# Kernel optimization log

Measured on AMD Instinct MI355X. Metric: run time of the kernel, lower is better.

The kernel has to match this reference:

```python
import jax, jax.numpy as jnp
import numpy as np

N_LAYERS = 6
D_MODEL = 512
D_FFN = 2048
N_STATE = 64
KSIZE = 31
BATCH = 8
SEQ = 2048
IN_SIZE = 80


def _ln(x, g, b, eps=1e-5):
    m = jnp.mean(x, axis=-1, keepdims=True)
    v = jnp.mean((x - m) ** 2, axis=-1, keepdims=True)
    return (x - m) * jax.lax.rsqrt(v + eps) * g + b


def _ffn(x, g, b, w1, b1, w2, b2):
    # LayerNorm -> Linear(D->F) -> GELU -> Linear(F->D)  (PositionalwiseFeedForward)
    h = jax.nn.gelu(_ln(x, g, b) @ w1 + b1)
    return h @ w2 + b2


def _dss(x, lam_re, lam_im, c_re, c_im, d_skip, log_dt, w_out, b_out):
    # Diagonal state-space (DSS-EXP): generate length-T kernel from diagonal poles,
    # apply causal conv via FFT, skip D*u, GELU, GLU output projection.
    Bx, T, H = x.shape
    dt = jnp.exp(log_dt)
    lam = -jnp.exp(lam_re) + 1j * lam_im                        # [N] stable poles (Re<0)
    P = jnp.exp(lam[:, None] * (dt * jnp.arange(T))[None, :])   # [N, T]
    C = c_re + 1j * c_im                                        # [H, N]
    kern = jnp.einsum('hn,nt->ht', C, P).real * dt              # [H, T]
    u = x.transpose(0, 2, 1)                                    # [B, H, T]
    n = 2 * T
    y = jnp.fft.irfft(jnp.fft.rfft(u, n=n) * jnp.fft.rfft(kern, n=n), n=n)[..., :T]
    y = y + d_skip[None, :, None] * u
    y = jax.nn.gelu(y.transpose(0, 2, 1))                       # [B, T, H]
    z = y @ w_out + b_out                                       # [B, T, 2H]
    a, g = jnp.split(z, 2, axis=-1)
    return a * jax.nn.sigmoid(g)                                # GLU


def _conv_module(x, g1, b1, bw, bb, dw, db, g2, b2, lw, lb):
    # LN -> 1x1 conv to 2D + GLU -> depthwise conv (SAME, k=31) -> LN -> GELU -> Linear
    y = _ln(x, g1, b1)
    y = y @ bw.T + bb                                           # [B, T, 2D]
    a, g = jnp.split(y, 2, axis=-1)
    y = a * jax.nn.sigmoid(g)                                   # GLU over channels
    yc = y.transpose(0, 2, 1)                                   # [B, D, T]
    yc = jax.lax.conv_general_dilated(
        yc, dw[:, None, :], (1,), 'SAME',
        feature_group_count=yc.shape[1],
        dimension_numbers=('NCH', 'OIH', 'NCH'))
    yc = yc + db[None, :, None]
    y = jax.nn.gelu(_ln(yc.transpose(0, 2, 1), g2, b2))
    return y @ lw.T + lb


def _forward(src, speaker_embs, src_w, src_b,
             ffn1_ln_g, ffn1_ln_b, ffn1_w1, ffn1_b1, ffn1_w2, ffn1_b2,
             norm1_g, norm1_b,
             lam_re, lam_im, c_re, c_im, ssm_d, log_dt, dss_out_w, dss_out_b,
             conv_ln_g, conv_ln_b, bneck_w, bneck_b, dw_w, dw_b,
             conv_ln2_g, conv_ln2_b, conv_lin_w, conv_lin_b,
             ffn2_ln_g, ffn2_ln_b, ffn2_w1, ffn2_b1, ffn2_w2, ffn2_b2,
             norm2_g, norm2_b, final_g, final_b):
    x = src @ src_w + src_b                                     # custom_src_module Linear
    for i in range(N_LAYERS):
        x = x + 0.5 * _ffn(x, ffn1_ln_g[i], ffn1_ln_b[i], ffn1_w1[i], ffn1_b1[i], ffn1_w2[i], ffn1_b2[i])
        skip = x
        x = _ln(x, norm1_g[i], norm1_b[i])
        x = _dss(x, lam_re[i], lam_im[i], c_re[i], c_im[i], ssm_d[i], log_dt[i], dss_out_w[i], dss_out_b[i])
        x = x + skip
        x = x + _conv_module(x, conv_ln_g[i], conv_ln_b[i], bneck_w[i], bneck_b[i], dw_w[i], dw_b[i],
                             conv_ln2_g[i], conv_ln2_b[i], conv_lin_w[i], conv_lin_b[i])
        x = _ln(x + 0.5 * _ffn(x, ffn2_ln_g[i], ffn2_ln_b[i], ffn2_w1[i], ffn2_b1[i], ffn2_w2[i], ffn2_b2[i]),
                norm2_g[i], norm2_b[i])
    x = _ln(x, final_g, final_b, eps=1e-6)
    return x + speaker_embs


def setup_inputs() -> dict:
    key = jax.random.key(0)
    ks = iter(jax.random.split(key, 64))
    def rn(shape, s=0.02):
        return (jax.random.normal(next(ks), shape) * s).astype(jnp.float32)
    L, D, F, N, K = N_LAYERS, D_MODEL, D_FFN, N_STATE, KSIZE
    return dict(
        src=jax.random.normal(next(ks), (BATCH, SEQ, IN_SIZE), dtype=jnp.float32),
        speaker_embs=jax.random.normal(next(ks), (BATCH, 1, D), dtype=jnp.float32),
        src_w=rn((IN_SIZE, D)), src_b=jnp.zeros((D,), jnp.float32),
        ffn1_ln_g=jnp.ones((L, D), jnp.float32), ffn1_ln_b=jnp.zeros((L, D), jnp.float32),
        ffn1_w1=rn((L, D, F)), ffn1_b1=jnp.zeros((L, F), jnp.float32),
        ffn1_w2=rn((L, F, D)), ffn1_b2=jnp.zeros((L, D), jnp.float32),
        norm1_g=jnp.ones((L, D), jnp.float32), norm1_b=jnp.zeros((L, D), jnp.float32),
        lam_re=rn((L, N), 0.5), lam_im=rn((L, N), 3.0),
        c_re=rn((L, D, N), 0.1), c_im=rn((L, D, N), 0.1),
        ssm_d=rn((L, D), 1.0), log_dt=jnp.full((L,), float(np.log(0.01)), jnp.float32),
        dss_out_w=rn((L, D, 2 * D)), dss_out_b=jnp.zeros((L, 2 * D), jnp.float32),
        conv_ln_g=jnp.ones((L, D), jnp.float32), conv_ln_b=jnp.zeros((L, D), jnp.float32),
        bneck_w=rn((L, 2 * D, D)), bneck_b=jnp.zeros((L, 2 * D), jnp.float32),
        dw_w=rn((L, D, K), 0.1), dw_b=jnp.zeros((L, D), jnp.float32),
        conv_ln2_g=jnp.ones((L, D), jnp.float32), conv_ln2_b=jnp.zeros((L, D), jnp.float32),
        conv_lin_w=rn((L, D, D)), conv_lin_b=jnp.zeros((L, D), jnp.float32),
        ffn2_ln_g=jnp.ones((L, D), jnp.float32), ffn2_ln_b=jnp.zeros((L, D), jnp.float32),
        ffn2_w1=rn((L, D, F)), ffn2_b1=jnp.zeros((L, F), jnp.float32),
        ffn2_w2=rn((L, F, D)), ffn2_b2=jnp.zeros((L, D), jnp.float32),
        norm2_g=jnp.ones((L, D), jnp.float32), norm2_b=jnp.zeros((L, D), jnp.float32),
        final_g=jnp.ones((D,), jnp.float32), final_b=jnp.zeros((D,), jnp.float32),
    )


def reference(src, speaker_embs, src_w, src_b,
              ffn1_ln_g, ffn1_ln_b, ffn1_w1, ffn1_b1, ffn1_w2, ffn1_b2,
              norm1_g, norm1_b,
              lam_re, lam_im, c_re, c_im, ssm_d, log_dt, dss_out_w, dss_out_b,
              conv_ln_g, conv_ln_b, bneck_w, bneck_b, dw_w, dw_b,
              conv_ln2_g, conv_ln2_b, conv_lin_w, conv_lin_b,
              ffn2_ln_g, ffn2_ln_b, ffn2_w1, ffn2_b1, ffn2_w2, ffn2_b2,
              norm2_g, norm2_b, final_g, final_b):
    return _forward(src, speaker_embs, src_w, src_b,
                    ffn1_ln_g, ffn1_ln_b, ffn1_w1, ffn1_b1, ffn1_w2, ffn1_b2,
                    norm1_g, norm1_b,
                    lam_re, lam_im, c_re, c_im, ssm_d, log_dt, dss_out_w, dss_out_b,
                    conv_ln_g, conv_ln_b, bneck_w, bneck_b, dw_w, dw_b,
                    conv_ln2_g, conv_ln2_b, conv_lin_w, conv_lin_b,
                    ffn2_ln_g, ffn2_ln_b, ffn2_w1, ffn2_b1, ffn2_w2, ffn2_b2,
                    norm2_g, norm2_b, final_g, final_b)
```

## Files before the change

kernel.cpp:

```cpp
#include <hip/hip_runtime.h>
#include <hip/hip_bf16.h>
#include <stdint.h>


#define NL 6
#define TT 2048
#define BB 8
#define DD 512
#define FF 2048
#define ROWS (BB*TT)

typedef __attribute__((ext_vector_type(4))) float f32x4;
typedef __attribute__((ext_vector_type(8))) short s16x8;

#define DEVI __device__ __forceinline__

DEVI float bf2f(uint32_t u) { union { uint32_t i; float f; } v; v.i = u << 16; return v.f; }
DEVI uint16_t f2bf(float f) {
    union { float f; uint32_t i; } v; v.f = f;
    uint32_t x = v.i;
    return (uint16_t)((x + 0x7fffu + ((x >> 16) & 1u)) >> 16);
}
DEVI float gelu_f(float x) {
    float x2 = x * x;
    float z  = x * fmaf(x2, 0.07135481627f, 1.5957691216f);
    return x * __builtin_amdgcn_rcpf(1.0f + __expf(-z));
}
DEVI float sigm(float x) { return __builtin_amdgcn_rcpf(1.0f + __expf(-x)); }

DEVI void gload16(const uint16_t* g, uint16_t* l) {
    __builtin_amdgcn_global_load_lds((const __attribute__((address_space(1))) void*)g,
                                     (__attribute__((address_space(3))) void*)l, 16, 0, 0);
}

__global__ void k_wtrans(const float* __restrict__ src, uint16_t* __restrict__ dst,
                         int K, int N) {
    __shared__ float tile[32][33];
    int l = blockIdx.z;
    const float* s = src + (size_t)l * K * N;
    uint16_t*    d = dst + (size_t)l * N * K;
    int n0 = blockIdx.x * 32, k0 = blockIdx.y * 32;
    int tx = threadIdx.x, ty = threadIdx.y;
#pragma unroll
    for (int i = 0; i < 4; i++) {
        int k = k0 + ty + i * 8;
        tile[ty + i * 8][tx] = s[(size_t)k * N + n0 + tx];
    }
    __syncthreads();
#pragma unroll
    for (int i = 0; i < 4; i++) {
        int n = n0 + ty + i * 8;
        d[(size_t)n * K + k0 + tx] = f2bf(tile[tx][ty + i * 8]);
    }
}
__global__ void k_wcvt(const float* __restrict__ src, uint16_t* __restrict__ dst, int n) {
    int i = blockIdx.x * 256 + threadIdx.x;
    if (i < n) dst[i] = f2bf(src[i]);
}
__global__ void k_dwt(const float* __restrict__ dw, float* __restrict__ dwt) {
    int i = blockIdx.x * 256 + threadIdx.x;
    int tot = NL * DD * 31;
    if (i >= tot) return;
    int l = i / (DD * 31), r = i % (DD * 31), d = r / 31, k = r % 31;
    dwt[(size_t)l * 31 * DD + k * DD + d] = dw[i];
}
__global__ void k_srcpad(const float* __restrict__ src, uint16_t* __restrict__ dst) {
    int i = blockIdx.x * 256 + threadIdx.x;
    if (i >= ROWS * 128) return;
    int r = i >> 7, c = i & 127;
    dst[i] = (c < 80) ? f2bf(src[(size_t)r * 80 + c]) : (uint16_t)0;
}
__global__ void k_wsrcpad(const float* __restrict__ w, uint16_t* __restrict__ dst) {
    int i = blockIdx.x * 256 + threadIdx.x;
    if (i >= DD * 128) return;
    int n = i >> 7, k = i & 127;
    dst[i] = (k < 80) ? f2bf(w[(size_t)k * DD + n]) : (uint16_t)0;
}

template <int MODE>
__global__ void k_ln(const float* __restrict__ in, void* __restrict__ outp,
                     const float* __restrict__ gam, const float* __restrict__ bet,
                     const float* __restrict__ spk, float eps) {
    int row  = blockIdx.x * 4 + (threadIdx.x >> 6);
    int lane = threadIdx.x & 63;
    const float* x = in + (size_t)row * DD;
    float4 a0 = *(const float4*)&x[lane * 4];
    float4 a1 = *(const float4*)&x[256 + lane * 4];
    float v[8] = {a0.x, a0.y, a0.z, a0.w, a1.x, a1.y, a1.z, a1.w};
    float s = 0.f, q = 0.f;
#pragma unroll
    for (int i = 0; i < 8; i++) { s += v[i]; q += v[i] * v[i]; }
#pragma unroll
    for (int m = 1; m < 64; m <<= 1) { s += __shfl_xor(s, m); q += __shfl_xor(q, m); }
    float mean = s * (1.0f / 512.0f);
    float var  = fmaxf(q * (1.0f / 512.0f) - mean * mean, 0.0f);
    float inv  = rsqrtf(var + eps);
    float4 g0 = *(const float4*)&gam[lane * 4];
    float4 g1 = *(const float4*)&gam[256 + lane * 4];
    float4 b0 = *(const float4*)&bet[lane * 4];
    float4 b1 = *(const float4*)&bet[256 + lane * 4];
    float gv[8] = {g0.x, g0.y, g0.z, g0.w, g1.x, g1.y, g1.z, g1.w};
    float bv[8] = {b0.x, b0.y, b0.z, b0.w, b1.x, b1.y, b1.z, b1.w};
    float y[8];
#pragma unroll
    for (int i = 0; i < 8; i++) y[i] = (v[i] - mean) * inv * gv[i] + bv[i];
    uint16_t* o = (uint16_t*)outp + (size_t)row * DD;
    uint2 p0, p1;
    p0.x = (uint32_t)f2bf(y[0]) | ((uint32_t)f2bf(y[1]) << 16);
    p0.y = (uint32_t)f2bf(y[2]) | ((uint32_t)f2bf(y[3]) << 16);
    p1.x = (uint32_t)f2bf(y[4]) | ((uint32_t)f2bf(y[5]) << 16);
    p1.y = (uint32_t)f2bf(y[6]) | ((uint32_t)f2bf(y[7]) << 16);
    *(uint2*)&o[lane * 4]       = p0;
    *(uint2*)&o[256 + lane * 4] = p1;
}

template <int M2>
__global__ void k_ln2(const float* __restrict__ in, float* __restrict__ X,
                      void* __restrict__ out2,
                      const float* __restrict__ g1, const float* __restrict__ b1,
                      const float* __restrict__ g2, const float* __restrict__ b2,
                      const float* __restrict__ spk, float eps2) {
    int row  = blockIdx.x * 4 + (threadIdx.x >> 6);
    int lane = threadIdx.x & 63;
    const float* x = in + (size_t)row * DD;
    float4 a0 = *(const float4*)&x[lane * 4];
    float4 a1 = *(const float4*)&x[256 + lane * 4];
    float v[8] = {a0.x, a0.y, a0.z, a0.w, a1.x, a1.y, a1.z, a1.w};
    float s = 0.f, q = 0.f;
#pragma unroll
    for (int i = 0; i < 8; i++) { s += v[i]; q += v[i] * v[i]; }
#pragma unroll
    for (int m = 1; m < 64; m <<= 1) { s += __shfl_xor(s, m); q += __shfl_xor(q, m); }
    float mean = s * (1.0f / 512.0f);
    float var  = fmaxf(q * (1.0f / 512.0f) - mean * mean, 0.0f);
    float inv  = rsqrtf(var + 1e-5f);
    float4 g0 = *(const float4*)&g1[lane * 4];
    float4 g1v = *(const float4*)&g1[256 + lane * 4];
    float4 b0 = *(const float4*)&b1[lane * 4];
    float4 b1v = *(const float4*)&b1[256 + lane * 4];
    float gv[8] = {g0.x, g0.y, g0.z, g0.w, g1v.x, g1v.y, g1v.z, g1v.w};
    float bv[8] = {b0.x, b0.y, b0.z, b0.w, b1v.x, b1v.y, b1v.z, b1v.w};
    float y[8];
    float s2 = 0.f, q2 = 0.f;
#pragma unroll
    for (int i = 0; i < 8; i++) {
        y[i] = (v[i] - mean) * inv * gv[i] + bv[i];
        s2 += y[i]; q2 += y[i] * y[i];
    }
    if (M2 == 6) {
        float* xo = X + (size_t)row * DD;
        *(float4*)&xo[lane * 4]       = make_float4(y[0], y[1], y[2], y[3]);
        *(float4*)&xo[256 + lane * 4] = make_float4(y[4], y[5], y[6], y[7]);
    }
#pragma unroll
    for (int m = 1; m < 64; m <<= 1) { s2 += __shfl_xor(s2, m); q2 += __shfl_xor(q2, m); }
    float mean2 = s2 * (1.0f / 512.0f);
    float var2  = fmaxf(q2 * (1.0f / 512.0f) - mean2 * mean2, 0.0f);
    float inv2  = rsqrtf(var2 + eps2);
    float4 G0 = *(const float4*)&g2[lane * 4];
    float4 G1 = *(const float4*)&g2[256 + lane * 4];
    float4 B0 = *(const float4*)&b2[lane * 4];
    float4 B1v = *(const float4*)&b2[256 + lane * 4];
    float Gv[8] = {G0.x, G0.y, G0.z, G0.w, G1.x, G1.y, G1.z, G1.w};
    float Bv[8] = {B0.x, B0.y, B0.z, B0.w, B1v.x, B1v.y, B1v.z, B1v.w};
    float z[8];
#pragma unroll
    for (int i = 0; i < 8; i++) z[i] = (y[i] - mean2) * inv2 * Gv[i] + Bv[i];
    if (M2 == 6) {
        uint16_t* o = (uint16_t*)out2 + (size_t)row * DD;
        uint2 p0, p1;
        p0.x = (uint32_t)f2bf(z[0]) | ((uint32_t)f2bf(z[1]) << 16);
        p0.y = (uint32_t)f2bf(z[2]) | ((uint32_t)f2bf(z[3]) << 16);
        p1.x = (uint32_t)f2bf(z[4]) | ((uint32_t)f2bf(z[5]) << 16);
        p1.y = (uint32_t)f2bf(z[6]) | ((uint32_t)f2bf(z[7]) << 16);
        *(uint2*)&o[lane * 4]       = p0;
        *(uint2*)&o[256 + lane * 4] = p1;
    } else {
        const float* sp = spk + (size_t)(row >> 11) * DD;
        float4 s0 = *(const float4*)&sp[lane * 4];
        float4 s1 = *(const float4*)&sp[256 + lane * 4];
        float* o = (float*)out2 + (size_t)row * DD;
        *(float4*)&o[lane * 4]       = make_float4(z[0]+s0.x, z[1]+s0.y, z[2]+s0.z, z[3]+s0.w);
        *(float4*)&o[256 + lane * 4] = make_float4(z[4]+s1.x, z[5]+s1.y, z[6]+s1.z, z[7]+s1.w);
    }
}

__global__ void k_gluln(const uint16_t* __restrict__ H, float* __restrict__ X,
                        uint16_t* __restrict__ out,
                        const float* __restrict__ gam, const float* __restrict__ bet) {
    int row  = blockIdx.x * 4 + (threadIdx.x >> 6);
    int lane = threadIdx.x & 63;
    const uint16_t* hr = H + (size_t)row * 1024;
    uint2 ha0 = *(const uint2*)&hr[lane * 4];
    uint2 ha1 = *(const uint2*)&hr[256 + lane * 4];
    uint2 hg0 = *(const uint2*)&hr[512 + lane * 4];
    uint2 hg1 = *(const uint2*)&hr[768 + lane * 4];
    uint32_t aw[4] = {ha0.x, ha0.y, ha1.x, ha1.y};
    uint32_t gw[4] = {hg0.x, hg0.y, hg1.x, hg1.y};
    float* xr = X + (size_t)row * DD;
    float4 x0 = *(const float4*)&xr[lane * 4];
    float4 x1 = *(const float4*)&xr[256 + lane * 4];
    float xv[8] = {x0.x, x0.y, x0.z, x0.w, x1.x, x1.y, x1.z, x1.w};
    float v[8];
#pragma unroll
    for (int p = 0; p < 4; p++) {
        float a0 = bf2f(aw[p] & 0xffffu), a1 = bf2f(aw[p] >> 16);
        float g0 = bf2f(gw[p] & 0xffffu), g1 = bf2f(gw[p] >> 16);
        v[2*p]   = xv[2*p]   + a0 * sigm(g0);
        v[2*p+1] = xv[2*p+1] + a1 * sigm(g1);
    }
    *(float4*)&xr[lane * 4]       = make_float4(v[0], v[1], v[2], v[3]);
    *(float4*)&xr[256 + lane * 4] = make_float4(v[4], v[5], v[6], v[7]);
    float s = 0.f, q = 0.f;
#pragma unroll
    for (int i = 0; i < 8; i++) { s += v[i]; q += v[i] * v[i]; }
#pragma unroll
    for (int m = 1; m < 64; m <<= 1) { s += __shfl_xor(s, m); q += __shfl_xor(q, m); }
    float mean = s * (1.0f / 512.0f);
    float var  = fmaxf(q * (1.0f / 512.0f) - mean * mean, 0.0f);
    float inv  = rsqrtf(var + 1e-5f);
    float4 g0 = *(const float4*)&gam[lane * 4];
    float4 g1 = *(const float4*)&gam[256 + lane * 4];
    float4 b0 = *(const float4*)&bet[lane * 4];
    float4 b1 = *(const float4*)&bet[256 + lane * 4];
    float gv[8] = {g0.x, g0.y, g0.z, g0.w, g1.x, g1.y, g1.z, g1.w};
    float bv[8] = {b0.x, b0.y, b0.z, b0.w, b1.x, b1.y, b1.z, b1.w};
    uint16_t* o = out + (size_t)row * DD;
    uint2 p0, p1;
    float y0 = (v[0]-mean)*inv*gv[0]+bv[0], y1 = (v[1]-mean)*inv*gv[1]+bv[1];
    float y2 = (v[2]-mean)*inv*gv[2]+bv[2], y3 = (v[3]-mean)*inv*gv[3]+bv[3];
    float y4 = (v[4]-mean)*inv*gv[4]+bv[4], y5 = (v[5]-mean)*inv*gv[5]+bv[5];
    float y6 = (v[6]-mean)*inv*gv[6]+bv[6], y7 = (v[7]-mean)*inv*gv[7]+bv[7];
    p0.x = (uint32_t)f2bf(y0) | ((uint32_t)f2bf(y1) << 16);
    p0.y = (uint32_t)f2bf(y2) | ((uint32_t)f2bf(y3) << 16);
    p1.x = (uint32_t)f2bf(y4) | ((uint32_t)f2bf(y5) << 16);
    p1.y = (uint32_t)f2bf(y6) | ((uint32_t)f2bf(y7) << 16);
    *(uint2*)&o[lane * 4]       = p0;
    *(uint2*)&o[256 + lane * 4] = p1;
}

template <int MODE, int WM, int WN, int BN>
__global__ __launch_bounds__(512) void k_gemm2(
    const uint16_t* __restrict__ A, const uint16_t* __restrict__ Bt,
    const float* __restrict__ bias, int M, int N, int K,
    void* __restrict__ outp, float* __restrict__ X) {
    constexpr int BM = 256;
    constexpr int MR = BM / WM / 16;
    constexpr int NR = BN / WN / 16;
    constexpr int ABLK = (BM / 16) * 2;
    constexpr int BBLK = (BN / 16) * 2;
    constexpr int APW = ABLK / 8;
    constexpr int BPW = BBLK / 8;
    __shared__ __align__(16) uint16_t As[2][ABLK * 512];
    __shared__ __align__(16) uint16_t Bs[2][BBLK * 512];
    int tid = threadIdx.x;
    int wave = tid >> 6, lane = tid & 63;
    int l15 = lane & 15, l16 = lane >> 4;
    int wr = wave / WN, wc = wave % WN;
    int m0 = blockIdx.x * BM, n0 = blockIdx.y * BN;

    const uint16_t* srcA[APW];
    const uint16_t* srcB[BPW];
#pragma unroll
    for (int p = 0; p < APW; p++) {
        int bi = wave * APW + p, rb = bi >> 1, ks = bi & 1;
        srcA[p] = A + (size_t)(m0 + rb * 16 + l15) * K + ks * 32 + l16 * 8;
    }
#pragma unroll
    for (int p = 0; p < BPW; p++) {
        int bi = wave * BPW + p, rb = bi >> 1, ks = bi & 1;
        srcB[p] = Bt + (size_t)(n0 + rb * 16 + l15) * K + ks * 32 + l16 * 8;
    }

    f32x4 acc[MR][NR];
#pragma unroll
    for (int i = 0; i < MR; i++)
#pragma unroll
        for (int j = 0; j < NR; j++) acc[i][j] = (f32x4){0.f, 0.f, 0.f, 0.f};

#pragma unroll
    for (int p = 0; p < APW; p++) gload16(srcA[p], &As[0][(wave * APW + p) * 512]);
#pragma unroll
    for (int p = 0; p < BPW; p++) gload16(srcB[p], &Bs[0][(wave * BPW + p) * 512]);
    __syncthreads();

    int nk = K >> 6;
    for (int it = 0; it < nk; ++it) {
        int cur = it & 1;
        if (it + 1 < nk) {
            int kt = (it + 1) << 6;
#pragma unroll
            for (int p = 0; p < APW; p++)
                gload16(srcA[p] + kt, &As[cur ^ 1][(wave * APW + p) * 512]);
#pragma unroll
            for (int p = 0; p < BPW; p++)
                gload16(srcB[p] + kt, &Bs[cur ^ 1][(wave * BPW + p) * 512]);
        }
#pragma unroll
        for (int s = 0; s < 2; s++) {
            s16x8 af[MR], bfr[NR];
#pragma unroll
            for (int i = 0; i < MR; i++)
                af[i] = *(const s16x8*)&As[cur][((wr * MR + i) * 2 + s) * 512 + lane * 8];
#pragma unroll
            for (int j = 0; j < NR; j++)
                bfr[j] = *(const s16x8*)&Bs[cur][((wc * NR + j) * 2 + s) * 512 + lane * 8];
#pragma unroll
            for (int i = 0; i < MR; i++)
#pragma unroll
                for (int j = 0; j < NR; j++)
                    acc[i][j] = __builtin_amdgcn_mfma_f32_16x16x32_bf16(af[i], bfr[j], acc[i][j], 0, 0, 0);
        }
        __syncthreads();
    }
#pragma unroll
    for (int i = 0; i < MR; i++) {
#pragma unroll
        for (int j = 0; j < NR; j++) {
            int gcol = n0 + wc * NR * 16 + j * 16 + l15;
            float bv = bias[gcol];
#pragma unroll
            for (int q = 0; q < 4; q++) {
                int grow = m0 + wr * MR * 16 + i * 16 + l16 * 4 + q;
                float v = acc[i][j][q] + bv;
                if (MODE == 0) {
                    ((uint16_t*)outp)[(size_t)grow * N + gcol] = f2bf(gelu_f(v));
                } else if (MODE == 1) {
                    ((uint16_t*)outp)[(size_t)grow * N + gcol] = f2bf(v);
                } else if (MODE == 2) {
                    X[(size_t)grow * DD + gcol] += 0.5f * v;
                } else if (MODE == 3) {
                    X[(size_t)grow * DD + gcol] += v;
                } else if (MODE == 4) {
                    ((float*)outp)[(size_t)grow * DD + gcol] =
                        X[(size_t)grow * DD + gcol] + 0.5f * v;
                } else {
                    X[(size_t)grow * DD + gcol] = v;
                }
            }
        }
    }
}

__global__ void k_tpose(const uint16_t* __restrict__ in, uint16_t* __restrict__ out,
                        int R, int C) {
    __shared__ uint16_t tile[32][33];
    size_t boff = (size_t)blockIdx.z * R * C;
    int c0 = blockIdx.x * 32, r0 = blockIdx.y * 32;
    int tx = threadIdx.x, ty = threadIdx.y;
#pragma unroll
    for (int i = 0; i < 4; i++)
        tile[ty + i * 8][tx] = in[boff + (size_t)(r0 + ty + i * 8) * C + c0 + tx];
    __syncthreads();
#pragma unroll
    for (int i = 0; i < 4; i++)
        out[boff + (size_t)(c0 + ty + i * 8) * R + r0 + tx] = tile[tx][ty + i * 8];
}

__global__ __launch_bounds__(64) void k_phiprep(
        const float* __restrict__ lam_re, const float* __restrict__ lam_im,
        const float* __restrict__ log_dt, uint16_t* __restrict__ PHI,
        float* __restrict__ A64f) {
    int l = blockIdx.x, n = threadIdx.x;
    float dt = expf(log_dt[l]);
    float lr = lam_re[l * 64 + n], li = lam_im[l * 64 + n];
    float mag = expf(-expf(lr) * dt), th = li * dt;
    float Are = mag * __cosf(th), Aim = mag * __sinf(th);
    float Pre = 1.f, Pim = 0.f;
    uint16_t* ph = PHI + (size_t)l * 8192;
    for (int tau = 0; tau < 64; tau++) {
        int s = 63 - tau;
        ph[n * 64 + s]        = f2bf(Pre);
        ph[(64 + n) * 64 + s] = f2bf(Pim);
        float nr = Pre * Are - Pim * Aim;
        float ni = Pre * Aim + Pim * Are;
        Pre = nr; Pim = ni;
    }
    A64f[l * 128 + 2 * n]     = Pre;
    A64f[l * 128 + 2 * n + 1] = Pim;
}

__global__ __launch_bounds__(64) void k_gprep(
        const float* __restrict__ lam_re, const float* __restrict__ lam_im,
        const float* __restrict__ c_re, const float* __restrict__ c_im,
        const float* __restrict__ ssm_d, const float* __restrict__ log_dt,
        int l, uint16_t* __restrict__ G) {
    int h = blockIdx.x, n = threadIdx.x;
    __shared__ float klds[64];
    float dt = expf(log_dt[l]);
    float lr = lam_re[l * 64 + n], li = lam_im[l * 64 + n];
    float mag = expf(-expf(lr) * dt), th = li * dt;
    float Are = mag * __cosf(th), Aim = mag * __sinf(th);
    float Cre = c_re[(size_t)l * DD * 64 + h * 64 + n];
    float Cim = c_im[(size_t)l * DD * 64 + h * 64 + n];
    uint16_t* Gh = G + (size_t)h * 64 * 192;
    float Pre = 1.f, Pim = 0.f;
    for (int r = 0; r < 64; r++) {
        float t = Cre * Pre - Cim * Pim;
        float s = t;
        s += __shfl_xor(s, 1);  s += __shfl_xor(s, 2);  s += __shfl_xor(s, 4);
        s += __shfl_xor(s, 8);  s += __shfl_xor(s, 16); s += __shfl_xor(s, 32);
        if (n == 0) klds[r] = dt * s;
        float nr = Pre * Are - Pim * Aim;
        float ni = Pre * Aim + Pim * Are;
        float wre = dt * (Cre * nr - Cim * ni);
        float wim = dt * (Cre * ni + Cim * nr);
        Gh[r * 192 + 64 + n]  = f2bf(wre);
        Gh[r * 192 + 128 + n] = f2bf(-wim);
        Pre = nr; Pim = ni;
    }
    __syncthreads();
    float dh = ssm_d[l * DD + h];
    for (int r = 0; r < 64; r++) {
        int c = n;
        float val = (c < r) ? klds[r - c] : (c == r ? klds[0] + dh : 0.f);
        Gh[r * 192 + c] = f2bf(val);
    }
}

__global__ __launch_bounds__(256) void k_pass1(
        const uint16_t* __restrict__ u, const uint16_t* __restrict__ PHI,
        uint16_t* __restrict__ E) {
    __shared__ __align__(16) uint16_t Phs[128 * 72];
    int tid = threadIdx.x;
    for (int v = tid; v < 1024; v += 256) {
        int row = v >> 3, kb = v & 7;
        *(s16x8*)&Phs[row * 72 + kb * 8] = *(const s16x8*)&PHI[row * 64 + kb * 8];
    }
    __syncthreads();
    int wave = tid >> 6, lane = tid & 63;
    int l15 = lane & 15, l16 = lane >> 4;
    int m0 = (wave & 1) * 64;
    int colbase = blockIdx.x * 128 + (wave >> 1) * 64;
    f32x4 acc[4][4];
#pragma unroll
    for (int i = 0; i < 4; i++)
#pragma unroll
        for (int j = 0; j < 4; j++) acc[i][j] = (f32x4){0.f, 0.f, 0.f, 0.f};
#pragma unroll
    for (int kt = 0; kt < 64; kt += 32) {
        s16x8 a[4], b[4];
#pragma unroll
        for (int i = 0; i < 4; i++)
            a[i] = *(const s16x8*)&Phs[(m0 + i * 16 + l15) * 72 + kt + l16 * 8];
#pragma unroll
        for (int j = 0; j < 4; j++)
            b[j] = *(const s16x8*)(u + (size_t)(colbase + j * 16 + l15) * 64 + kt + l16 * 8);
#pragma unroll
        for (int i = 0; i < 4; i++)
#pragma unroll
            for (int j = 0; j < 4; j++)
                acc[i][j] = __builtin_amdgcn_mfma_f32_16x16x32_bf16(a[i], b[j], acc[i][j], 0, 0, 0);
    }
#pragma unroll
    for (int i = 0; i < 4; i++)
#pragma unroll
        for (int j = 0; j < 4; j++) {
            int col = colbase + j * 16 + l15;
            int r0  = m0 + i * 16 + l16 * 4;
            uint32_t p0 = (uint32_t)f2bf(acc[i][j][0]) | ((uint32_t)f2bf(acc[i][j][1]) << 16);
            uint32_t p1 = (uint32_t)f2bf(acc[i][j][2]) | ((uint32_t)f2bf(acc[i][j][3]) << 16);
            *(uint2*)&E[(size_t)col * 128 + r0] = make_uint2(p0, p1);
        }
}

__global__ void k_pass2(const uint16_t* __restrict__ E, const float* __restrict__ A64f,
                        int l, uint16_t* __restrict__ Sp) {
    int gid = blockIdx.x * 256 + threadIdx.x;
    int n = gid & 63, bh = gid >> 6;
    int b = bh >> 9, h = bh & 511;
    float2 A = *(const float2*)&A64f[l * 128 + 2 * n];
    float Sre = 0.f, Sim = 0.f;
    const uint16_t* Eb = E + (size_t)bh * 32 * 128;
    uint16_t* So = Sp + (size_t)h * 32768 + (size_t)b * 32 * 128;
    for (int i = 0; i < 32; i++) {
        So[i * 128 + n]      = f2bf(Sre);
        So[i * 128 + 64 + n] = f2bf(Sim);
        float er = bf2f((uint32_t)Eb[i * 128 + n]);
        float ei = bf2f((uint32_t)Eb[i * 128 + 64 + n]);
        float nr = A.x * Sre - A.y * Sim + er;
        float ni = A.x * Sim + A.y * Sre + ei;
        Sre = nr; Sim = ni;
    }
}

__global__ __launch_bounds__(256) void k_pass3(
        const uint16_t* __restrict__ G, const uint16_t* __restrict__ u,
        const uint16_t* __restrict__ Sp, uint16_t* __restrict__ Y) {
    __shared__ __align__(16) uint16_t Gs[64 * 200];
    int h = blockIdx.x, tid = threadIdx.x;
    for (int v = tid; v < 1536; v += 256) {
        int row = v / 24, kb = v % 24;
        *(s16x8*)&Gs[row * 200 + kb * 8] = *(const s16x8*)&G[(size_t)h * 12288 + row * 192 + kb * 8];
    }
    __syncthreads();
    int wave = tid >> 6, lane = tid & 63;
    int l15 = lane & 15, l16 = lane >> 4;
    int wn = wave * 64;
    const uint16_t* uh = u + (size_t)h * TT;
    const uint16_t* sh = Sp + (size_t)h * 32768;
    f32x4 acc[4][4];
#pragma unroll
    for (int i = 0; i < 4; i++)
#pragma unroll
        for (int j = 0; j < 4; j++) acc[i][j] = (f32x4){0.f, 0.f, 0.f, 0.f};
#pragma unroll
    for (int kt = 0; kt < 192; kt += 32) {
        s16x8 a[4], b[4];
#pragma unroll
        for (int i = 0; i < 4; i++)
            a[i] = *(const s16x8*)&Gs[(i * 16 + l15) * 200 + kt + l16 * 8];
#pragma unroll
        for (int j = 0; j < 4; j++) {
            int col = wn + j * 16 + l15;
            const uint16_t* src;
            if (kt < 64)
                src = uh + (size_t)(col >> 5) * (DD * TT) + (col & 31) * 64 + kt + l16 * 8;
            else
                src = sh + (size_t)col * 128 + (kt - 64) + l16 * 8;
            b[j] = *(const s16x8*)src;
        }
#pragma unroll
        for (int i = 0; i < 4; i++)
#pragma unroll
            for (int j = 0; j < 4; j++)
                acc[i][j] = __builtin_amdgcn_mfma_f32_16x16x32_bf16(a[i], b[j], acc[i][j], 0, 0, 0);
    }
#pragma unroll
    for (int i = 0; i < 4; i++)
#pragma unroll
        for (int j = 0; j < 4; j++) {
            int col = wn + j * 16 + l15;
            int r0  = i * 16 + l16 * 4;
            uint16_t* dst = Y + (size_t)(col >> 5) * (DD * TT) + (size_t)h * TT + (col & 31) * 64 + r0;
            uint32_t p0 = (uint32_t)f2bf(acc[i][j][0]) | ((uint32_t)f2bf(acc[i][j][1]) << 16);
            uint32_t p1 = (uint32_t)f2bf(acc[i][j][2]) | ((uint32_t)f2bf(acc[i][j][3]) << 16);
            *(uint2*)&dst[0] = make_uint2(p0, p1);
        }
}

__global__ void k_tgelu(const uint16_t* __restrict__ y, uint16_t* __restrict__ out) {
    __shared__ uint16_t tile[32][33];
    int b = blockIdx.z;
    int t0 = blockIdx.x * 32, h0 = blockIdx.y * 32;
    int tx = threadIdx.x, ty = threadIdx.y;
    const uint16_t* yb = y + (size_t)b * DD * TT;
#pragma unroll
    for (int i = 0; i < 4; i++) {
        int h = h0 + ty + i * 8;
        tile[ty + i * 8][tx] = f2bf(gelu_f(bf2f((uint32_t)yb[(size_t)h * TT + t0 + tx])));
    }
    __syncthreads();
    uint16_t* ob = out + (size_t)b * TT * DD;
#pragma unroll
    for (int i = 0; i < 4; i++) {
        int t = t0 + ty + i * 8;
        ob[(size_t)t * DD + h0 + tx] = tile[tx][ty + i * 8];
    }
}

__global__ void k_glu(const uint16_t* __restrict__ z, uint16_t* __restrict__ out) {
    int i = blockIdx.x * 256 + threadIdx.x;
    int r = i >> 8;
    int c = (i & 255) * 2;
    uint32_t av = *(const uint32_t*)&z[(size_t)r * 1024 + c];
    uint32_t gv = *(const uint32_t*)&z[(size_t)r * 1024 + 512 + c];
    float a0 = bf2f(av & 0xffffu), a1 = bf2f(av >> 16);
    float g0 = bf2f(gv & 0xffffu), g1 = bf2f(gv >> 16);
    float v0 = a0 * sigm(g0), v1 = a1 * sigm(g1);
    uint32_t p = (uint32_t)f2bf(v0) | ((uint32_t)f2bf(v1) << 16);
    *(uint32_t*)&out[(size_t)r * DD + c] = p;
}

__global__ __launch_bounds__(256) void k_dwln(
        const uint16_t* __restrict__ in, const float* __restrict__ dwt,
        const float* __restrict__ db, const float* __restrict__ gam,
        const float* __restrict__ bet, uint16_t* __restrict__ out) {
    __shared__ __align__(16) uint16_t xs[34 * 512];
    __shared__ float red[4][4][2];
    int tid = threadIdx.x;
    int t0 = (blockIdx.x & 511) * 4;
    int b  = blockIdx.x >> 9;
    const uint16_t* ib = in + (size_t)b * TT * DD;
    for (int v = tid; v < 34 * 64; v += 256) {
        int row = v >> 6, seg = v & 63;
        int tj = t0 - 15 + row;
        uint4 val = make_uint4(0, 0, 0, 0);
        if (tj >= 0 && tj < TT) val = *(const uint4*)&ib[(size_t)tj * DD + seg * 8];
        *(uint4*)&xs[row * 512 + seg * 8] = val;
    }
    __syncthreads();
    int d = tid * 2;
    int wave = tid >> 6, lane = tid & 63;
    float a0[4], a1[4];
    float bv0 = db[d], bv1 = db[d + 1];
#pragma unroll
    for (int o = 0; o < 4; o++) { a0[o] = bv0; a1[o] = bv1; }
#pragma unroll
    for (int k = 0; k < 31; k++) {
        float2 w = *(const float2*)&dwt[k * DD + d];
#pragma unroll
        for (int o = 0; o < 4; o++) {
            uint32_t v = *(const uint32_t*)&xs[(o + k) * 512 + d];
            a0[o] = fmaf(bf2f(v & 0xffffu), w.x, a0[o]);
            a1[o] = fmaf(bf2f(v >> 16), w.y, a1[o]);
        }
    }
#pragma unroll
    for (int o = 0; o < 4; o++) {
        float ss = a0[o] + a1[o];
        float qq = a0[o] * a0[o] + a1[o] * a1[o];
#pragma unroll
        for (int m = 1; m < 64; m <<= 1) { ss += __shfl_xor(ss, m); qq += __shfl_xor(qq, m); }
        if (lane == 0) { red[o][wave][0] = ss; red[o][wave][1] = qq; }
    }
    __syncthreads();
    float g0 = gam[d], g1 = gam[d + 1], be0 = bet[d], be1 = bet[d + 1];
#pragma unroll
    for (int o = 0; o < 4; o++) {
        float s = red[o][0][0] + red[o][1][0] + red[o][2][0] + red[o][3][0];
        float q = red[o][0][1] + red[o][1][1] + red[o][2][1] + red[o][3][1];
        float mean = s * (1.0f / 512.0f);
        float var  = fmaxf(q * (1.0f / 512.0f) - mean * mean, 0.0f);
        float inv  = rsqrtf(var + 1e-5f);
        float y0 = gelu_f((a0[o] - mean) * inv * g0 + be0);
        float y1 = gelu_f((a1[o] - mean) * inv * g1 + be1);
        uint32_t p = (uint32_t)f2bf(y0) | ((uint32_t)f2bf(y1) << 16);
        *(uint32_t*)&out[((size_t)b * TT + t0 + o) * DD + d] = p;
    }
}

extern "C" void kernel_launch(void* const* d_in, const int* in_sizes, int n_in,
                              void* d_out, int out_size, void* d_ws, size_t ws_size,
                              hipStream_t stream) {
    const float* src        = (const float*)d_in[0];
    const float* speaker    = (const float*)d_in[1];
    const float* src_w      = (const float*)d_in[2];
    const float* src_b      = (const float*)d_in[3];
    const float* ffn1_ln_g  = (const float*)d_in[4];
    const float* ffn1_ln_b  = (const float*)d_in[5];
    const float* ffn1_w1    = (const float*)d_in[6];
    const float* ffn1_b1    = (const float*)d_in[7];
    const float* ffn1_w2    = (const float*)d_in[8];
    const float* ffn1_b2    = (const float*)d_in[9];
    const float* norm1_g    = (const float*)d_in[10];
    const float* norm1_b    = (const float*)d_in[11];
    const float* lam_re     = (const float*)d_in[12];
    const float* lam_im     = (const float*)d_in[13];
    const float* c_re       = (const float*)d_in[14];
    const float* c_im       = (const float*)d_in[15];
    const float* ssm_d      = (const float*)d_in[16];
    const float* log_dt     = (const float*)d_in[17];
    const float* dss_out_w  = (const float*)d_in[18];
    const float* dss_out_b  = (const float*)d_in[19];
    const float* conv_ln_g  = (const float*)d_in[20];
    const float* conv_ln_b  = (const float*)d_in[21];
    const float* bneck_w    = (const float*)d_in[22];
    const float* bneck_b    = (const float*)d_in[23];
    const float* dw_w       = (const float*)d_in[24];
    const float* dw_b       = (const float*)d_in[25];
    const float* conv_ln2_g = (const float*)d_in[26];
    const float* conv_ln2_b = (const float*)d_in[27];
    const float* conv_lin_w = (const float*)d_in[28];
    const float* conv_lin_b = (const float*)d_in[29];
    const float* ffn2_ln_g  = (const float*)d_in[30];
    const float* ffn2_ln_b  = (const float*)d_in[31];
    const float* ffn2_w1    = (const float*)d_in[32];
    const float* ffn2_b1    = (const float*)d_in[33];
    const float* ffn2_w2    = (const float*)d_in[34];
    const float* ffn2_b2    = (const float*)d_in[35];
    const float* norm2_g    = (const float*)d_in[36];
    const float* norm2_b    = (const float*)d_in[37];
    const float* final_g    = (const float*)d_in[38];
    const float* final_b    = (const float*)d_in[39];
    (void)in_sizes; (void)n_in; (void)out_size; (void)ws_size;

    uint8_t* ws = (uint8_t*)d_ws;
    float*    X   = (float*)   (ws + 0);
    float*    F0  = (float*)   (ws + 33554432);
    uint16_t* B1  = (uint16_t*)(ws + 67108864);
    uint16_t* B2  = (uint16_t*)(ws + 83886080);
    uint16_t* B3  = (uint16_t*)(ws + 100663296);
    uint16_t* H   = (uint16_t*)(ws + 117440512);
    uint16_t* Wf1a= (uint16_t*)(ws + 184549376);
    uint16_t* Wf1b= (uint16_t*)(ws + 197132288);
    uint16_t* Wds = (uint16_t*)(ws + 209715200);
    uint16_t* Wbn = (uint16_t*)(ws + 216006656);
    uint16_t* Wcl = (uint16_t*)(ws + 222298112);
    uint16_t* Wf2a= (uint16_t*)(ws + 225443840);
    uint16_t* Wf2b= (uint16_t*)(ws + 238026752);
    float*    DWT = (float*)   (ws + 250609664);
    uint16_t* PHI = (uint16_t*)(ws + 250990592);
    float*    A64f= (float*)   (ws + 251088896);

    uint16_t* GBUF = B1;
    uint16_t* SPK  = (uint16_t*)F0;
    uint16_t* EBUF = H;
    uint16_t* SRCB = B3;
    uint16_t* WSRC = B2;

    dim3 tb(32, 8);
    k_wtrans<<<dim3(FF/32, DD/32, NL), tb, 0, stream>>>(ffn1_w1, Wf1a, DD, FF);
    k_wtrans<<<dim3(DD/32, FF/32, NL), tb, 0, stream>>>(ffn1_w2, Wf1b, FF, DD);
    k_wtrans<<<dim3(1024/32, DD/32, NL), tb, 0, stream>>>(dss_out_w, Wds, DD, 1024);
    k_wcvt<<<(NL*1024*DD + 255)/256, 256, 0, stream>>>(bneck_w, Wbn, NL*1024*DD);
    k_wcvt<<<(NL*DD*DD + 255)/256, 256, 0, stream>>>(conv_lin_w, Wcl, NL*DD*DD);
    k_wtrans<<<dim3(FF/32, DD/32, NL), tb, 0, stream>>>(ffn2_w1, Wf2a, DD, FF);
    k_wtrans<<<dim3(DD/32, FF/32, NL), tb, 0, stream>>>(ffn2_w2, Wf2b, FF, DD);
    k_dwt<<<(NL*DD*31 + 255)/256, 256, 0, stream>>>(dw_w, DWT);
    k_phiprep<<<NL, 64, 0, stream>>>(lam_re, lam_im, log_dt, PHI, A64f);
    k_srcpad<<<(ROWS*128 + 255)/256, 256, 0, stream>>>(src, SRCB);
    k_wsrcpad<<<(DD*128 + 255)/256, 256, 0, stream>>>(src_w, WSRC);

    k_gemm2<5,4,2,128><<<dim3(64, 4), 512, 0, stream>>>(SRCB, WSRC, src_b, ROWS, DD, 128, nullptr, X);
    k_ln<0><<<4096, 256, 0, stream>>>(X, B1, ffn1_ln_g, ffn1_ln_b, nullptr, 1e-5f);

    for (int l = 0; l < NL; l++) {
        k_gemm2<0,2,4,256><<<dim3(64, 8), 512, 0, stream>>>(B1, Wf1a + (size_t)l*FF*DD, ffn1_b1 + l*FF,
                                                            ROWS, FF, DD, H, nullptr);
        k_gemm2<2,4,2,128><<<dim3(64, 4), 512, 0, stream>>>(H, Wf1b + (size_t)l*DD*FF, ffn1_b2 + l*DD,
                                                            ROWS, DD, FF, nullptr, X);
        k_ln<0><<<4096, 256, 0, stream>>>(X, B1, norm1_g + l*DD, norm1_b + l*DD, nullptr, 1e-5f);
        k_tpose<<<dim3(DD/32, TT/32, BB), tb, 0, stream>>>(B1, B2, TT, DD);
        k_gprep<<<DD, 64, 0, stream>>>(lam_re, lam_im, c_re, c_im, ssm_d, log_dt, l, GBUF);
        k_pass1<<<1024, 256, 0, stream>>>(B2, PHI + (size_t)l*8192, EBUF);
        k_pass2<<<1024, 256, 0, stream>>>(EBUF, A64f, l, SPK);
        k_pass3<<<DD, 256, 0, stream>>>(GBUF, B2, SPK, B3);
        k_tgelu<<<dim3(TT/32, DD/32, BB), tb, 0, stream>>>(B3, B1);
        k_gemm2<1,2,4,256><<<dim3(64, 4), 512, 0, stream>>>(B1, Wds + (size_t)l*1024*DD, dss_out_b + l*1024,
                                                            ROWS, 1024, DD, H, nullptr);
        k_gluln<<<4096, 256, 0, stream>>>(H, X, B1, conv_ln_g + l*DD, conv_ln_b + l*DD);
        k_gemm2<1,2,4,256><<<dim3(64, 4), 512, 0, stream>>>(B1, Wbn + (size_t)l*1024*DD, bneck_b + l*1024,
                                                            ROWS, 1024, DD, H, nullptr);
        k_glu<<<ROWS, 256, 0, stream>>>(H, B2);
        k_dwln<<<BB*512, 256, 0, stream>>>(B2, DWT + (size_t)l*31*DD, dw_b + l*DD,
                                           conv_ln2_g + l*DD, conv_ln2_b + l*DD, B1);
        k_gemm2<3,4,2,128><<<dim3(64, 4), 512, 0, stream>>>(B1, Wcl + (size_t)l*DD*DD, conv_lin_b + l*DD,
                                                            ROWS, DD, DD, nullptr, X);
        k_ln<0><<<4096, 256, 0, stream>>>(X, B1, ffn2_ln_g + l*DD, ffn2_ln_b + l*DD, nullptr, 1e-5f);
        k_gemm2<0,2,4,256><<<dim3(64, 8), 512, 0, stream>>>(B1, Wf2a + (size_t)l*FF*DD, ffn2_b1 + l*FF,
                                                            ROWS, FF, DD, H, nullptr);
        k_gemm2<4,4,2,128><<<dim3(64, 4), 512, 0, stream>>>(H, Wf2b + (size_t)l*DD*FF, ffn2_b2 + l*DD,
                                                            ROWS, DD, FF, F0, X);
        if (l < NL - 1) {
            k_ln2<6><<<4096, 256, 0, stream>>>(F0, X, B1, norm2_g + l*DD, norm2_b + l*DD,
                                               ffn1_ln_g + (l+1)*DD, ffn1_ln_b + (l+1)*DD,
                                               nullptr, 1e-5f);
        } else {
            k_ln2<7><<<4096, 256, 0, stream>>>(F0, nullptr, d_out, norm2_g + l*DD, norm2_b + l*DD,
                                               final_g, final_b, speaker, 1e-6f);
        }
    }
}
```

Before: 3.403 ms.

## Rewrite GEMM with triple-buffered K=32 pipeline and XCD-aware block swizzle

Replaces the double-buffered K=64 GEMM with a triple-buffered K=32 pipeline. It uses explicit vmcnt waits and a single barrier per step, so global loads run two stages ahead of the MFMA work. Work-group IDs are remapped across the eight XCDs so neighbouring tiles share L2, and launch bounds now request two blocks per CU. The warp layout is fixed at 2x4 with 8 M-fragments per wave, which raises register pressure. The hand-set vmcnt counts depend on how many loads each stage issues and are easy to get wrong.

Result: slower. 3.657 ms (+7.5%).

```diff
diff --git a/kernel.cpp b/kernel.cpp
--- a/kernel.cpp
+++ b/kernel.cpp
@@ -239,37 +239,43 @@
     *(uint2*)&o[256 + lane * 4] = p1;
 }
 
-template <int MODE, int WM, int WN, int BN>
-__global__ __launch_bounds__(512) void k_gemm2(
+template <int MODE, int BN>
+__global__ __launch_bounds__(512, 2) void k_gemm3(
     const uint16_t* __restrict__ A, const uint16_t* __restrict__ Bt,
     const float* __restrict__ bias, int M, int N, int K,
     void* __restrict__ outp, float* __restrict__ X) {
-    constexpr int BM = 256;
-    constexpr int MR = BM / WM / 16;
-    constexpr int NR = BN / WN / 16;
-    constexpr int ABLK = (BM / 16) * 2;
-    constexpr int BBLK = (BN / 16) * 2;
-    constexpr int APW = ABLK / 8;
+    constexpr int MR = 8;
+    constexpr int NR = BN / 64;
+    constexpr int ABLK = 16;
+    constexpr int BBLK = BN / 16;
+    constexpr int APW = 2;
     constexpr int BPW = BBLK / 8;
-    __shared__ __align__(16) uint16_t As[2][ABLK * 512];
-    __shared__ __align__(16) uint16_t Bs[2][BBLK * 512];
+    constexpr int LV  = APW + BPW;
+    __shared__ __align__(16) uint16_t As[3][ABLK * 512];
+    __shared__ __align__(16) uint16_t Bs[3][BBLK * 512];
     int tid = threadIdx.x;
     int wave = tid >> 6, lane = tid & 63;
     int l15 = lane & 15, l16 = lane >> 4;
-    int wr = wave / WN, wc = wave % WN;
-    int m0 = blockIdx.x * BM, n0 = blockIdx.y * BN;
+    int wr = wave >> 2, wc = wave & 3;
+
+    int nwg = gridDim.x;
+    int q8  = nwg >> 3;
+    int wg  = (blockIdx.x & 7) * q8 + (blockIdx.x >> 3);
+    int nbx = M >> 8;
+    int bx = wg % nbx, by = wg / nbx;
+    int m0 = bx * 256, n0 = by * BN;
 
     const uint16_t* srcA[APW];
     const uint16_t* srcB[BPW];
 #pragma unroll
     for (int p = 0; p < APW; p++) {
-        int bi = wave * APW + p, rb = bi >> 1, ks = bi & 1;
-        srcA[p] = A + (size_t)(m0 + rb * 16 + l15) * K + ks * 32 + l16 * 8;
+        int bi = wave * APW + p;
+        srcA[p] = A + (size_t)(m0 + bi * 16 + l15) * K + l16 * 8;
     }
 #pragma unroll
     for (int p = 0; p < BPW; p++) {
-        int bi = wave * BPW + p, rb = bi >> 1, ks = bi & 1;
-        srcB[p] = Bt + (size_t)(n0 + rb * 16 + l15) * K + ks * 32 + l16 * 8;
+        int bi = wave * BPW + p;
+        srcB[p] = Bt + (size_t)(n0 + bi * 16 + l15) * K + l16 * 8;
     }
 
     f32x4 acc[MR][NR];
@@ -278,40 +284,43 @@
 #pragma unroll
         for (int j = 0; j < NR; j++) acc[i][j] = (f32x4){0.f, 0.f, 0.f, 0.f};
 
-#pragma unroll
-    for (int p = 0; p < APW; p++) gload16(srcA[p], &As[0][(wave * APW + p) * 512]);
-#pragma unroll
-    for (int p = 0; p < BPW; p++) gload16(srcB[p], &Bs[0][(wave * BPW + p) * 512]);
-    __syncthreads();
-
-    int nk = K >> 6;
-    for (int it = 0; it < nk; ++it) {
-        int cur = it & 1;
-        if (it + 1 < nk) {
-            int kt = (it + 1) << 6;
-#pragma unroll
-            for (int p = 0; p < APW; p++)
-                gload16(srcA[p] + kt, &As[cur ^ 1][(wave * APW + p) * 512]);
-#pragma unroll
-            for (int p = 0; p < BPW; p++)
-                gload16(srcB[p] + kt, &Bs[cur ^ 1][(wave * BPW + p) * 512]);
+    auto STAGE = [&](int tt) {
+        int b = tt % 3;
+        int kof = tt << 5;
+#pragma unroll
+        for (int p = 0; p < APW; p++)
+            gload16(srcA[p] + kof, &As[b][(wave * APW + p) * 512]);
+#pragma unroll
+        for (int p = 0; p < BPW; p++)
+            gload16(srcB[p] + kof, &Bs[b][(wave * BPW + p) * 512]);
+    };
+
+    int nk = K >> 5;
+    STAGE(0);
+    STAGE(1);
+    for (int t = 0; t < nk; ++t) {
+        if (t + 1 < nk) {
+            if (LV == 4) asm volatile("s_waitcnt vmcnt(4)" ::: "memory");
+            else         asm volatile("s_waitcnt vmcnt(3)" ::: "memory");
+        } else {
+            asm volatile("s_waitcnt vmcnt(0)" ::: "memory");
         }
-#pragma unroll
-        for (int s = 0; s < 2; s++) {
-            s16x8 af[MR], bfr[NR];
-#pragma unroll
-            for (int i = 0; i < MR; i++)
-                af[i] = *(const s16x8*)&As[cur][((wr * MR + i) * 2 + s) * 512 + lane * 8];
+        __builtin_amdgcn_s_barrier();
+        asm volatile("" ::: "memory");
+        if (t + 2 < nk) STAGE(t + 2);
+        int buf = t % 3;
+        s16x8 af[MR], bfr[NR];
+#pragma unroll
+        for (int i = 0; i < MR; i++)
+            af[i] = *(const s16x8*)&As[buf][(wr * MR + i) * 512 + lane * 8];
+#pragma unroll
+        for (int j = 0; j < NR; j++)
+            bfr[j] = *(const s16x8*)&Bs[buf][(wc * NR + j) * 512 + lane * 8];
+#pragma unroll
+        for (int i = 0; i < MR; i++)
 #pragma unroll
             for (int j = 0; j < NR; j++)
-                bfr[j] = *(const s16x8*)&Bs[cur][((wc * NR + j) * 2 + s) * 512 + lane * 8];
-#pragma unroll
-            for (int i = 0; i < MR; i++)
-#pragma unroll
-                for (int j = 0; j < NR; j++)
-                    acc[i][j] = __builtin_amdgcn_mfma_f32_16x16x32_bf16(af[i], bfr[j], acc[i][j], 0, 0, 0);
-        }
-        __syncthreads();
+                acc[i][j] = __builtin_amdgcn_mfma_f32_16x16x32_bf16(af[i], bfr[j], acc[i][j], 0, 0, 0);
     }
 #pragma unroll
     for (int i = 0; i < MR; i++) {
@@ -712,14 +721,14 @@
     k_srcpad<<<(ROWS*128 + 255)/256, 256, 0, stream>>>(src, SRCB);
     k_wsrcpad<<<(DD*128 + 255)/256, 256, 0, stream>>>(src_w, WSRC);
 
-    k_gemm2<5,4,2,128><<<dim3(64, 4), 512, 0, stream>>>(SRCB, WSRC, src_b, ROWS, DD, 128, nullptr, X);
+    k_gemm3<5,128><<<256, 512, 0, stream>>>(SRCB, WSRC, src_b, ROWS, DD, 128, nullptr, X);
     k_ln<0><<<4096, 256, 0, stream>>>(X, B1, ffn1_ln_g, ffn1_ln_b, nullptr, 1e-5f);
 
     for (int l = 0; l < NL; l++) {
-        k_gemm2<0,2,4,256><<<dim3(64, 8), 512, 0, stream>>>(B1, Wf1a + (size_t)l*FF*DD, ffn1_b1 + l*FF,
-                                                            ROWS, FF, DD, H, nullptr);
-        k_gemm2<2,4,2,128><<<dim3(64, 4), 512, 0, stream>>>(H, Wf1b + (size_t)l*DD*FF, ffn1_b2 + l*DD,
-                                                            ROWS, DD, FF, nullptr, X);
+        k_gemm3<0,256><<<512, 512, 0, stream>>>(B1, Wf1a + (size_t)l*FF*DD, ffn1_b1 + l*FF,
+                                                ROWS, FF, DD, H, nullptr);
+        k_gemm3<2,128><<<256, 512, 0, stream>>>(H, Wf1b + (size_t)l*DD*FF, ffn1_b2 + l*DD,
+                                                ROWS, DD, FF, nullptr, X);
         k_ln<0><<<4096, 256, 0, stream>>>(X, B1, norm1_g + l*DD, norm1_b + l*DD, nullptr, 1e-5f);
         k_tpose<<<dim3(DD/32, TT/32, BB), tb, 0, stream>>>(B1, B2, TT, DD);
         k_gprep<<<DD, 64, 0, stream>>>(lam_re, lam_im, c_re, c_im, ssm_d, log_dt, l, GBUF);
@@ -727,21 +736,21 @@
         k_pass2<<<1024, 256, 0, stream>>>(EBUF, A64f, l, SPK);
         k_pass3<<<DD, 256, 0, stream>>>(GBUF, B2, SPK, B3);
         k_tgelu<<<dim3(TT/32, DD/32, BB), tb, 0, stream>>>(B3, B1);
-        k_gemm2<1,2,4,256><<<dim3(64, 4), 512, 0, stream>>>(B1, Wds + (size_t)l*1024*DD, dss_out_b + l*1024,
-                                                            ROWS, 1024, DD, H, nullptr);
+        k_gemm3<1,256><<<256, 512, 0, stream>>>(B1, Wds + (size_t)l*1024*DD, dss_out_b + l*1024,
+                                                ROWS, 1024, DD, H, nullptr);
         k_gluln<<<4096, 256, 0, stream>>>(H, X, B1, conv_ln_g + l*DD, conv_ln_b + l*DD);
-        k_gemm2<1,2,4,256><<<dim3(64, 4), 512, 0, stream>>>(B1, Wbn + (size_t)l*1024*DD, bneck_b + l*1024,
-                                                            ROWS, 1024, DD, H, nullptr);
+        k_gemm3<1,256><<<256, 512, 0, stream>>>(B1, Wbn + (size_t)l*1024*DD, bneck_b + l*1024,
+                                                ROWS, 1024, DD, H, nullptr);
         k_glu<<<ROWS, 256, 0, stream>>>(H, B2);
         k_dwln<<<BB*512, 256, 0, stream>>>(B2, DWT + (size_t)l*31*DD, dw_b + l*DD,
                                            conv_ln2_g + l*DD, conv_ln2_b + l*DD, B1);
-        k_gemm2<3,4,2,128><<<dim3(64, 4), 512, 0, stream>>>(B1, Wcl + (size_t)l*DD*DD, conv_lin_b + l*DD,
-                                                            ROWS, DD, DD, nullptr, X);
+        k_gemm3<3,128><<<256, 512, 0, stream>>>(B1, Wcl + (size_t)l*DD*DD, conv_lin_b + l*DD,
+                                                ROWS, DD, DD, nullptr, X);
         k_ln<0><<<4096, 256, 0, stream>>>(X, B1, ffn2_ln_g + l*DD, ffn2_ln_b + l*DD, nullptr, 1e-5f);
-        k_gemm2<0,2,4,256><<<dim3(64, 8), 512, 0, stream>>>(B1, Wf2a + (size_t)l*FF*DD, ffn2_b1 + l*FF,
-                                                            ROWS, FF, DD, H, nullptr);
-        k_gemm2<4,4,2,128><<<dim3(64, 4), 512, 0, stream>>>(H, Wf2b + (size_t)l*DD*FF, ffn2_b2 + l*DD,
-                                                            ROWS, DD, FF, F0, X);
+        k_gemm3<0,256><<<512, 512, 0, stream>>>(B1, Wf2a + (size_t)l*FF*DD, ffn2_b1 + l*FF,
+                                                ROWS, FF, DD, H, nullptr);
+        k_gemm3<4,128><<<256, 512, 0, stream>>>(H, Wf2b + (size_t)l*DD*FF, ffn2_b2 + l*DD,
+                                                ROWS, DD, FF, F0, X);
         if (l < NL - 1) {
             k_ln2<6><<<4096, 256, 0, stream>>>(F0, X, B1, norm2_g + l*DD, norm2_b + l*DD,
                                                ffn1_ln_g + (l+1)*DD, ffn1_ln_b + (l+1)*DD,
```
